# Kernel tuning notes

Hardware: AMD Instinct MI355X
Metric: run time of the kernel (lower is better)

## Reference

```python
import jax, jax.numpy as jnp
import numpy as np

N_NODES = 100000


def gcn_conv(x, W, b, src, dst, num_nodes):
    # PyG GCNConv: add self-loops, symmetric normalization, x @ W, scatter-add, + b
    xw = x @ W  # [N, out]
    loop = jnp.arange(num_nodes, dtype=src.dtype)
    s = jnp.concatenate([src, loop])  # message source j
    d = jnp.concatenate([dst, loop])  # aggregation target i
    deg = jax.ops.segment_sum(jnp.ones_like(d, dtype=xw.dtype), d, num_segments=num_nodes)
    dis = jnp.where(deg > 0, jax.lax.rsqrt(deg), 0.0)  # D^{-1/2}
    norm = dis[s] * dis[d]  # [E+N]
    msg = norm[:, None] * xw[s]  # gather + scale
    out = jax.ops.segment_sum(msg, d, num_segments=num_nodes)  # scatter-add
    return out + b


def setup_inputs() -> dict:
    key = jax.random.key(0)
    k1, k2, k3, k4 = jax.random.split(key, 4)
    F, H, E = 64, 64, 1250000
    x = jax.random.normal(k1, (N_NODES, F), dtype=jnp.float32)
    edge_index = jax.random.randint(k2, (2, E), 0, N_NODES, dtype=jnp.int64)
    W1 = jax.random.normal(k3, (F, H), dtype=jnp.float32) * (1.0 / np.sqrt(F))
    b1 = jnp.zeros((H,), dtype=jnp.float32)
    W2 = jax.random.normal(k4, (H, F), dtype=jnp.float32) * (1.0 / np.sqrt(H))
    b2 = jnp.zeros((F,), dtype=jnp.float32)
    return {"x": x, "edge_index": edge_index, "W1": W1, "b1": b1, "W2": W2, "b2": b2}


def reference(x, edge_index, W1, b1, W2, b2):
    src, dst = edge_index[0], edge_index[1]
    h = gcn_conv(x, W1, b1, src, dst, N_NODES)
    h = jax.nn.relu(h)
    out = gcn_conv(h, W2, b2, src, dst, N_NODES)
    return out
```

## Files before the change

### kernel.cpp

```cpp
#include <hip/hip_runtime.h>

#define NN    100000
#define F     64
#define NBUCK 391
#define CAPB  4096
#define TILE  4096
#define NBLKG 782
#define G1A   400

#define O_CURSOR 0
#define O_ROWPTR 512
#define O_DEG    100864
#define O_DIS    201216
#define O_PACKED 301568
#define O_SRT    1903104
#define O_AH     3504768
#define O_BH     6704768
#define O_W2F    9904768

typedef __attribute__((ext_vector_type(8))) short bf16x8;
typedef __attribute__((ext_vector_type(4))) float f32x4;

__device__ __forceinline__ unsigned bf_rne(float x) {
    unsigned u = __float_as_uint(x);
    return (u + 0x7FFFu + ((u >> 16) & 1u)) >> 16;
}
__device__ __forceinline__ unsigned pack2(float lo, float hi) {
    return bf_rne(lo) | (bf_rne(hi) << 16);
}
__device__ __forceinline__ float lo_f(unsigned u) { return __uint_as_float(u << 16); }
__device__ __forceinline__ float hi_f(unsigned u) { return __uint_as_float(u & 0xFFFF0000u); }

struct BpSmem {
    int hist[NBUCK], lofs[NBUCK], gbase[NBUCK], lcur[NBUCK];
    int wsum[8];
    unsigned stage[TILE];
    unsigned short sbuck[TILE];
};
union KSmem {
    BpSmem bp;
    unsigned w1f[16][64][4];
};
struct NsSmem {
    int h[256], lcur[256], wsum[4];
    int stage[CAPB];
};
union K2Smem {
    NsSmem ns;
    unsigned w1f[16][64][4];
};
struct K3Smem {
    unsigned w2f[16][64][4];
    unsigned hbuf[16 * 32];
    float dis_s[16];
};

__device__ __forceinline__ void binpack_body(const int* __restrict__ src,
                                             const int* __restrict__ dst, int E,
                                             int* __restrict__ cursor,
                                             unsigned* __restrict__ packed,
                                             int bid, BpSmem& sm) {
    int t  = threadIdx.x;
    int t0 = bid * TILE;
    int n  = min(TILE, E - t0);

    if (t < NBUCK) sm.hist[t] = 0;
    __syncthreads();
    int d_r[8], s_r[8];
#pragma unroll
    for (int it = 0; it < 8; ++it) {
        int i = t + it * 512;
        if (i < n) {
            d_r[it] = dst[t0 + i];
            s_r[it] = src[t0 + i];
            atomicAdd(&sm.hist[d_r[it] >> 8], 1);
        }
    }
    __syncthreads();
    int lane = t & 63, w = t >> 6;
    int v = (t < NBUCK) ? sm.hist[t] : 0;
    int s = v;
#pragma unroll
    for (int off = 1; off < 64; off <<= 1) {
        int u = __shfl_up(s, off, 64);
        if (lane >= off) s += u;
    }
    if (lane == 63) sm.wsum[w] = s;
    __syncthreads();
    if (t == 0) {
        int run = 0;
#pragma unroll
        for (int i = 0; i < 8; ++i) { int c = sm.wsum[i]; sm.wsum[i] = run; run += c; }
    }
    __syncthreads();
    if (t < NBUCK) {
        int ex = s - v + sm.wsum[w];
        sm.lofs[t] = ex;
        sm.lcur[t] = ex;
        sm.gbase[t] = t * CAPB + (v ? atomicAdd(&cursor[t], v) : 0);
    }
    __syncthreads();
#pragma unroll
    for (int it = 0; it < 8; ++it) {
        int i = t + it * 512;
        if (i < n) {
            int d = d_r[it];
            int b = d >> 8;
            int p = atomicAdd(&sm.lcur[b], 1);
            sm.stage[p] = ((unsigned)s_r[it] << 8) | (unsigned)(d & 255);
            sm.sbuck[p] = (unsigned short)b;
        }
    }
    __syncthreads();
    for (int i = t; i < n; i += 512) {
        int b = sm.sbuck[i];
        packed[sm.gbase[b] + (i - sm.lofs[b])] = sm.stage[i];
    }
}

__device__ __forceinline__ void gemm_mfma_body(const float* __restrict__ X,
                                               const float* __restrict__ W,
                                               unsigned* __restrict__ Ah, int bid,
                                               unsigned (*w1f)[64][4]) {
    int t = threadIdx.x;
    for (int idx = t; idx < 4096; idx += 512) {
        int slot = idx >> 8;
        int ks   = (slot >> 1) & 1;
        int p    = slot & 1;
        int ct   = slot >> 2;
        int l    = (idx >> 2) & 63;
        int j    = idx & 3;
        int k    = 32 * ks + 8 * (l >> 4) + 2 * j;
        int col  = 16 * ct + (l & 15);
        float v0 = W[k * 64 + col];
        float v1 = W[(k + 1) * 64 + col];
        if (p) {
            v0 -= __uint_as_float(bf_rne(v0) << 16);
            v1 -= __uint_as_float(bf_rne(v1) << 16);
        }
        ((unsigned*)w1f)[idx] = pack2(v0, v1);
    }

    int lane = t & 63, wid = t >> 6;
    int g = lane >> 4;
    int wrow0 = bid * 128 + wid * 16;
    int wrow  = wrow0 + (lane & 15);
    bool valid = wrow < NN;
    const float* xp = X + (size_t)wrow * F + 8 * g;
    float4 fz = {0.f, 0.f, 0.f, 0.f};
    float4 f0 = valid ? *(const float4*)(xp)      : fz;
    float4 f1 = valid ? *(const float4*)(xp + 4)  : fz;
    float4 f2 = valid ? *(const float4*)(xp + 32) : fz;
    float4 f3 = valid ? *(const float4*)(xp + 36) : fz;
    __syncthreads();

    f32x4 ac0 = {0.f,0.f,0.f,0.f}, ac1 = ac0, ac2 = ac0, ac3 = ac0;
#pragma unroll
    for (int ks = 0; ks < 2; ++ks) {
        float4 u0 = ks ? f2 : f0;
        float4 u1 = ks ? f3 : f1;
        uint4 hw;
        hw.x = pack2(u0.x, u0.y);
        hw.y = pack2(u0.z, u0.w);
        hw.z = pack2(u1.x, u1.y);
        hw.w = pack2(u1.z, u1.w);
        uint4 lw;
        lw.x = pack2(u0.x - lo_f(hw.x), u0.y - hi_f(hw.x));
        lw.y = pack2(u0.z - lo_f(hw.y), u0.w - hi_f(hw.y));
        lw.z = pack2(u1.x - lo_f(hw.z), u1.y - hi_f(hw.z));
        lw.w = pack2(u1.z - lo_f(hw.w), u1.w - hi_f(hw.w));
        bf16x8 Ahi = __builtin_bit_cast(bf16x8, hw);
        bf16x8 Alo = __builtin_bit_cast(bf16x8, lw);
#pragma unroll
        for (int ct = 0; ct < 4; ++ct) {
            uint4 bh = *(const uint4*)&w1f[ct * 4 + ks * 2 + 0][lane][0];
            uint4 bl = *(const uint4*)&w1f[ct * 4 + ks * 2 + 1][lane][0];
            bf16x8 Bh_ = __builtin_bit_cast(bf16x8, bh);
            bf16x8 Bl_ = __builtin_bit_cast(bf16x8, bl);
            f32x4& ac = (ct == 0) ? ac0 : (ct == 1) ? ac1 : (ct == 2) ? ac2 : ac3;
            ac = __builtin_amdgcn_mfma_f32_16x16x32_bf16(Ahi, Bh_, ac, 0, 0, 0);
            ac = __builtin_amdgcn_mfma_f32_16x16x32_bf16(Alo, Bh_, ac, 0, 0, 0);
            ac = __builtin_amdgcn_mfma_f32_16x16x32_bf16(Ahi, Bl_, ac, 0, 0, 0);
        }
    }
#pragma unroll
    for (int ct = 0; ct < 4; ++ct) {
        f32x4 ac = (ct == 0) ? ac0 : (ct == 1) ? ac1 : (ct == 2) ? ac2 : ac3;
#pragma unroll
        for (int r = 0; r < 4; ++r) {
            float val = ac[r];
            float q = __shfl_xor(val, 1, 64);
            int row = wrow0 + 4 * g + r;
            if (!(lane & 1) && row < NN) {
                int colp = 8 * ct + ((lane & 15) >> 1);
                Ah[(size_t)row * 32 + colp] = pack2(val, q);
            }
        }
    }
}

__device__ __forceinline__ void w2prep_body(const float* __restrict__ W2,
                                            unsigned* __restrict__ w2f) {
    int t = threadIdx.x;
    for (int idx = t; idx < 4096; idx += 512) {
        int slot = idx >> 8;
        int ks   = (slot >> 1) & 1;
        int p    = slot & 1;
        int ct   = slot >> 2;
        int l    = (idx >> 2) & 63;
        int j    = idx & 3;
        int k    = 32 * ks + 8 * (l >> 4) + 2 * j;
        int col  = 16 * ct + (l & 15);
        float v0 = W2[k * 64 + col];
        float v1 = W2[(k + 1) * 64 + col];
        if (p) {
            v0 -= __uint_as_float(bf_rne(v0) << 16);
            v1 -= __uint_as_float(bf_rne(v1) << 16);
        }
        w2f[idx] = pack2(v0, v1);
    }
}

__device__ __forceinline__ void node_sort_body(const unsigned* __restrict__ packed,
                                               const int* __restrict__ cursor,
                                               int* __restrict__ row_ptr,
                                               int* __restrict__ deg,
                                               float* __restrict__ dis,
                                               int* __restrict__ srt,
                                               int b, NsSmem& sm) {
    int t = threadIdx.x;
    int nbase = b << 8;
    int nloc = min(256, NN - nbase);
    int beg = b * CAPB;
    int n = cursor[b];

    if (t < 256) sm.h[t] = 0;
    __syncthreads();
    unsigned p_r[8];
#pragma unroll
    for (int it = 0; it < 8; ++it) {
        int i = t + it * 512;
        if (i < n) {
            p_r[it] = packed[beg + i];
            atomicAdd(&sm.h[p_r[it] & 255u], 1);
        }
    }
    __syncthreads();
    int lane = t & 63, w = t >> 6;
    int v = 0, s = 0;
    if (t < 256) { v = sm.h[t]; s = v; }
#pragma unroll
    for (int off = 1; off < 64; off <<= 1) {
        int u = __shfl_up(s, off, 64);
        if (lane >= off) s += u;
    }
    if (t < 256 && lane == 63) sm.wsum[w] = s;
    __syncthreads();
    if (t == 0) {
        int run = 0;
#pragma unroll
        for (int i = 0; i < 4; ++i) { int c = sm.wsum[i]; sm.wsum[i] = run; run += c; }
    }
    __syncthreads();
    if (t < 256) {
        int e0 = s - v + sm.wsum[w];
        sm.lcur[t] = e0;
        if (t < nloc) {
            row_ptr[nbase + t] = beg + e0;
            deg[nbase + t]     = v;
            dis[nbase + t]     = rsqrtf((float)v + 1.0f);
        }
    }
    __syncthreads();
#pragma unroll
    for (int it = 0; it < 8; ++it) {
        int i = t + it * 512;
        if (i < n) {
            unsigned p = p_r[it];
            int pos = atomicAdd(&sm.lcur[p & 255u], 1);
            sm.stage[pos] = (int)(p >> 8);
        }
    }
    __syncthreads();
    for (int i = t; i < n; i += 512) srt[beg + i] = sm.stage[i];
}

__global__ __launch_bounds__(512) void pre_gemm1(const int* __restrict__ src,
                                                 const int* __restrict__ dst, int E,
                                                 int nbp, int* __restrict__ cursor,
                                                 unsigned* __restrict__ packed,
                                                 const float* __restrict__ X,
                                                 const float* __restrict__ W1,
                                                 unsigned* __restrict__ Ah,
                                                 const float* __restrict__ W2,
                                                 unsigned* __restrict__ w2f) {
    __shared__ KSmem sm;
    if ((int)blockIdx.x < nbp)
        binpack_body(src, dst, E, cursor, packed, blockIdx.x, sm.bp);
    else if ((int)blockIdx.x < nbp + G1A)
        gemm_mfma_body(X, W1, Ah, (int)blockIdx.x - nbp, sm.w1f);
    else
        w2prep_body(W2, w2f);
}

__global__ __launch_bounds__(512) void sort_gemm1(const unsigned* __restrict__ packed,
                                                  const int* __restrict__ cursor,
                                                  int* __restrict__ row_ptr,
                                                  int* __restrict__ deg,
                                                  float* __restrict__ dis,
                                                  int* __restrict__ srt,
                                                  const float* __restrict__ X,
                                                  const float* __restrict__ W1,
                                                  unsigned* __restrict__ Ah) {
    __shared__ K2Smem sm;
    if ((int)blockIdx.x < NBUCK)
        node_sort_body(packed, cursor, row_ptr, deg, dis, srt, blockIdx.x, sm.ns);
    else
        gemm_mfma_body(X, W1, Ah, G1A + (int)blockIdx.x - NBUCK, sm.w1f);
}

__global__ __launch_bounds__(256) void agg1_gemm2(const uint4* __restrict__ Ah4,
                                                  const int* __restrict__ row_ptr,
                                                  const int* __restrict__ deg,
                                                  const int* __restrict__ srt,
                                                  const float* __restrict__ dis,
                                                  const float* __restrict__ b1,
                                                  const unsigned* __restrict__ w2fg,
                                                  unsigned* __restrict__ Bh) {
    __shared__ K3Smem sm;
    int t = threadIdx.x;
#pragma unroll
    for (int i = 0; i < 4; ++i)
        ((uint4*)sm.w2f)[t + 256 * i] = ((const uint4*)w2fg)[t + 256 * i];

    int sub  = t & 7;
    int grp  = (t >> 3) & 1;
    int node = blockIdx.x * 16 + (t >> 4);
    int beg = row_ptr[node];
    int end = beg + deg[node];
    float di = dis[node];

    float a0, a1, a2, a3, a4, a5, a6, a7;
    uint4 su = Ah4[(size_t)node * 8 + sub];
    if (grp == 0) {
        a0 = di * lo_f(su.x); a1 = di * hi_f(su.x);
        a2 = di * lo_f(su.y); a3 = di * hi_f(su.y);
        a4 = di * lo_f(su.z); a5 = di * hi_f(su.z);
        a6 = di * lo_f(su.w); a7 = di * hi_f(su.w);
    } else {
        a0 = a1 = a2 = a3 = a4 = a5 = a6 = a7 = 0.f;
    }

    int j = beg + grp;
    for (; j + 6 < end; j += 8) {
        int s0 = srt[j], s1 = srt[j + 2], s2 = srt[j + 4], s3 = srt[j + 6];
        float d0 = dis[s0], d1 = dis[s1], d2 = dis[s2], d3 = dis[s3];
        uint4 g0 = Ah4[(size_t)s0 * 8 + sub];
        uint4 g1 = Ah4[(size_t)s1 * 8 + sub];
        uint4 g2 = Ah4[(size_t)s2 * 8 + sub];
        uint4 g3 = Ah4[(size_t)s3 * 8 + sub];
        a0 = fmaf(d0, lo_f(g0.x), fmaf(d1, lo_f(g1.x), fmaf(d2, lo_f(g2.x), fmaf(d3, lo_f(g3.x), a0))));
        a1 = fmaf(d0, hi_f(g0.x), fmaf(d1, hi_f(g1.x), fmaf(d2, hi_f(g2.x), fmaf(d3, hi_f(g3.x), a1))));
        a2 = fmaf(d0, lo_f(g0.y), fmaf(d1, lo_f(g1.y), fmaf(d2, lo_f(g2.y), fmaf(d3, lo_f(g3.y), a2))));
        a3 = fmaf(d0, hi_f(g0.y), fmaf(d1, hi_f(g1.y), fmaf(d2, hi_f(g2.y), fmaf(d3, hi_f(g3.y), a3))));
        a4 = fmaf(d0, lo_f(g0.z), fmaf(d1, lo_f(g1.z), fmaf(d2, lo_f(g2.z), fmaf(d3, lo_f(g3.z), a4))));
        a5 = fmaf(d0, hi_f(g0.z), fmaf(d1, hi_f(g1.z), fmaf(d2, hi_f(g2.z), fmaf(d3, hi_f(g3.z), a5))));
        a6 = fmaf(d0, lo_f(g0.w), fmaf(d1, lo_f(g1.w), fmaf(d2, lo_f(g2.w), fmaf(d3, lo_f(g3.w), a6))));
        a7 = fmaf(d0, hi_f(g0.w), fmaf(d1, hi_f(g1.w), fmaf(d2, hi_f(g2.w), fmaf(d3, hi_f(g3.w), a7))));
    }
    for (; j + 2 < end; j += 4) {
        int s0 = srt[j], s1 = srt[j + 2];
        float d0 = dis[s0], d1 = dis[s1];
        uint4 g0 = Ah4[(size_t)s0 * 8 + sub];
        uint4 g1 = Ah4[(size_t)s1 * 8 + sub];
        a0 = fmaf(d0, lo_f(g0.x), fmaf(d1, lo_f(g1.x), a0));
        a1 = fmaf(d0, hi_f(g0.x), fmaf(d1, hi_f(g1.x), a1));
        a2 = fmaf(d0, lo_f(g0.y), fmaf(d1, lo_f(g1.y), a2));
        a3 = fmaf(d0, hi_f(g0.y), fmaf(d1, hi_f(g1.y), a3));
        a4 = fmaf(d0, lo_f(g0.z), fmaf(d1, lo_f(g1.z), a4));
        a5 = fmaf(d0, hi_f(g0.z), fmaf(d1, hi_f(g1.z), a5));
        a6 = fmaf(d0, lo_f(g0.w), fmaf(d1, lo_f(g1.w), a6));
        a7 = fmaf(d0, hi_f(g0.w), fmaf(d1, hi_f(g1.w), a7));
    }
    for (; j < end; j += 2) {
        int s0 = srt[j];
        float d0 = dis[s0];
        uint4 g0 = Ah4[(size_t)s0 * 8 + sub];
        a0 = fmaf(d0, lo_f(g0.x), a0);
        a1 = fmaf(d0, hi_f(g0.x), a1);
        a2 = fmaf(d0, lo_f(g0.y), a2);
        a3 = fmaf(d0, hi_f(g0.y), a3);
        a4 = fmaf(d0, lo_f(g0.z), a4);
        a5 = fmaf(d0, hi_f(g0.z), a5);
        a6 = fmaf(d0, lo_f(g0.w), a6);
        a7 = fmaf(d0, hi_f(g0.w), a7);
    }
    a0 += __shfl_xor(a0, 8, 64); a1 += __shfl_xor(a1, 8, 64);
    a2 += __shfl_xor(a2, 8, 64); a3 += __shfl_xor(a3, 8, 64);
    a4 += __shfl_xor(a4, 8, 64); a5 += __shfl_xor(a5, 8, 64);
    a6 += __shfl_xor(a6, 8, 64); a7 += __shfl_xor(a7, 8, 64);

    float4 bb0 = ((const float4*)b1)[2 * sub];
    float4 bb1 = ((const float4*)b1)[2 * sub + 1];
    float o0 = fmaxf(fmaf(di, a0, bb0.x), 0.f);
    float o1 = fmaxf(fmaf(di, a1, bb0.y), 0.f);
    float o2 = fmaxf(fmaf(di, a2, bb0.z), 0.f);
    float o3 = fmaxf(fmaf(di, a3, bb0.w), 0.f);
    float o4 = fmaxf(fmaf(di, a4, bb1.x), 0.f);
    float o5 = fmaxf(fmaf(di, a5, bb1.y), 0.f);
    float o6 = fmaxf(fmaf(di, a6, bb1.z), 0.f);
    float o7 = fmaxf(fmaf(di, a7, bb1.w), 0.f);

    int node15 = t >> 4;
    if (!(t & 8)) {
        int unit = sub ^ (node15 & 7);
        uint4 hv;
        hv.x = pack2(o0, o1);
        hv.y = pack2(o2, o3);
        hv.z = pack2(o4, o5);
        hv.w = pack2(o6, o7);
        *(uint4*)&sm.hbuf[node15 * 32 + unit * 4] = hv;
        if (sub == 0) sm.dis_s[node15] = di;
    }
    __syncthreads();

    int lane = t & 63, ct = t >> 6;
    int row = lane & 15, g = lane >> 4;
    f32x4 acc = {0.f, 0.f, 0.f, 0.f};
#pragma unroll
    for (int ks = 0; ks < 2; ++ks) {
        int unit = (4 * ks + g) ^ (row & 7);
        uint4 araw = *(const uint4*)&sm.hbuf[row * 32 + unit * 4];
        uint4 bhr  = *(const uint4*)&sm.w2f[ct * 4 + ks * 2 + 0][lane][0];
        uint4 blr  = *(const uint4*)&sm.w2f[ct * 4 + ks * 2 + 1][lane][0];
        bf16x8 A  = __builtin_bit_cast(bf16x8, araw);
        bf16x8 Bh_ = __builtin_bit_cast(bf16x8, bhr);
        bf16x8 Bl_ = __builtin_bit_cast(bf16x8, blr);
        acc = __builtin_amdgcn_mfma_f32_16x16x32_bf16(A, Bh_, acc, 0, 0, 0);
        acc = __builtin_amdgcn_mfma_f32_16x16x32_bf16(A, Bl_, acc, 0, 0, 0);
    }
    int nbase16 = blockIdx.x * 16;
#pragma unroll
    for (int r = 0; r < 4; ++r) {
        int nd = 4 * g + r;
        float val = acc[r] * sm.dis_s[nd];
        float q = __shfl_xor(val, 1, 64);
        if (!(lane & 1)) {
            int colp = 8 * ct + ((lane & 15) >> 1);
            Bh[(size_t)(nbase16 + nd) * 32 + colp] = pack2(val, q);
        }
    }
}

__global__ __launch_bounds__(256) void agg_out(const uint4* __restrict__ Bs4,
                                               const int* __restrict__ row_ptr,
                                               const int* __restrict__ deg,
                                               const int* __restrict__ srt,
                                               const float* __restrict__ dis,
                                               const float* __restrict__ bias,
                                               float* __restrict__ outp) {
    int t = threadIdx.x;
    int sub  = t & 7;
    int grp  = (t >> 3) & 1;
    int node = blockIdx.x * 16 + (t >> 4);
    int beg = row_ptr[node];
    int end = beg + deg[node];
    float di = dis[node];

    float a0, a1, a2, a3, a4, a5, a6, a7;
    uint4 su = Bs4[(size_t)node * 8 + sub];
    if (grp == 0) {
        a0 = lo_f(su.x); a1 = hi_f(su.x);
        a2 = lo_f(su.y); a3 = hi_f(su.y);
        a4 = lo_f(su.z); a5 = hi_f(su.z);
        a6 = lo_f(su.w); a7 = hi_f(su.w);
    } else {
        a0 = a1 = a2 = a3 = a4 = a5 = a6 = a7 = 0.f;
    }

    int j = beg + grp;
    for (; j + 6 < end; j += 8) {
        int s0 = srt[j], s1 = srt[j + 2], s2 = srt[j + 4], s3 = srt[j + 6];
        uint4 g0 = Bs4[(size_t)s0 * 8 + sub];
        uint4 g1 = Bs4[(size_t)s1 * 8 + sub];
        uint4 g2 = Bs4[(size_t)s2 * 8 + sub];
        uint4 g3 = Bs4[(size_t)s3 * 8 + sub];
        a0 += (lo_f(g0.x) + lo_f(g1.x)) + (lo_f(g2.x) + lo_f(g3.x));
        a1 += (hi_f(g0.x) + hi_f(g1.x)) + (hi_f(g2.x) + hi_f(g3.x));
        a2 += (lo_f(g0.y) + lo_f(g1.y)) + (lo_f(g2.y) + lo_f(g3.y));
        a3 += (hi_f(g0.y) + hi_f(g1.y)) + (hi_f(g2.y) + hi_f(g3.y));
        a4 += (lo_f(g0.z) + lo_f(g1.z)) + (lo_f(g2.z) + lo_f(g3.z));
        a5 += (hi_f(g0.z) + hi_f(g1.z)) + (hi_f(g2.z) + hi_f(g3.z));
        a6 += (lo_f(g0.w) + lo_f(g1.w)) + (lo_f(g2.w) + lo_f(g3.w));
        a7 += (hi_f(g0.w) + hi_f(g1.w)) + (hi_f(g2.w) + hi_f(g3.w));
    }
    for (; j + 2 < end; j += 4) {
        int s0 = srt[j], s1 = srt[j + 2];
        uint4 g0 = Bs4[(size_t)s0 * 8 + sub];
        uint4 g1 = Bs4[(size_t)s1 * 8 + sub];
        a0 += lo_f(g0.x) + lo_f(g1.x);
        a1 += hi_f(g0.x) + hi_f(g1.x);
        a2 += lo_f(g0.y) + lo_f(g1.y);
        a3 += hi_f(g0.y) + hi_f(g1.y);
        a4 += lo_f(g0.z) + lo_f(g1.z);
        a5 += hi_f(g0.z) + hi_f(g1.z);
        a6 += lo_f(g0.w) + lo_f(g1.w);
        a7 += hi_f(g0.w) + hi_f(g1.w);
    }
    for (; j < end; j += 2) {
        int s0 = srt[j];
        uint4 g0 = Bs4[(size_t)s0 * 8 + sub];
        a0 += lo_f(g0.x); a1 += hi_f(g0.x);
        a2 += lo_f(g0.y); a3 += hi_f(g0.y);
        a4 += lo_f(g0.z); a5 += hi_f(g0.z);
        a6 += lo_f(g0.w); a7 += hi_f(g0.w);
    }
    a0 += __shfl_xor(a0, 8, 64); a1 += __shfl_xor(a1, 8, 64);
    a2 += __shfl_xor(a2, 8, 64); a3 += __shfl_xor(a3, 8, 64);
    a4 += __shfl_xor(a4, 8, 64); a5 += __shfl_xor(a5, 8, 64);
    a6 += __shfl_xor(a6, 8, 64); a7 += __shfl_xor(a7, 8, 64);

    float4 bb0 = ((const float4*)bias)[2 * sub];
    float4 bb1 = ((const float4*)bias)[2 * sub + 1];
    float4 o;
    if (grp == 0) {
        o.x = fmaf(di, a0, bb0.x);
        o.y = fmaf(di, a1, bb0.y);
        o.z = fmaf(di, a2, bb0.z);
        o.w = fmaf(di, a3, bb0.w);
        ((float4*)outp)[(size_t)node * 16 + 2 * sub] = o;
    } else {
        o.x = fmaf(di, a4, bb1.x);
        o.y = fmaf(di, a5, bb1.y);
        o.z = fmaf(di, a6, bb1.z);
        o.w = fmaf(di, a7, bb1.w);
        ((float4*)outp)[(size_t)node * 16 + 2 * sub + 1] = o;
    }
}

extern "C" void kernel_launch(void* const* d_in, const int* in_sizes, int n_in,
                              void* d_out, int out_size, void* d_ws, size_t ws_size,
                              hipStream_t stream) {
    const float* x  = (const float*)d_in[0];
    const int*   ei = (const int*)d_in[1];
    const float* W1 = (const float*)d_in[2];
    const float* b1 = (const float*)d_in[3];
    const float* W2 = (const float*)d_in[4];
    const float* b2 = (const float*)d_in[5];
    float* out = (float*)d_out;
    int E = in_sizes[1] / 2;
    const int* src = ei;
    const int* dst = ei + E;

    int*      ws_i    = (int*)d_ws;
    int*      cursor  = ws_i + O_CURSOR;
    int*      row_ptr = ws_i + O_ROWPTR;
    int*      deg     = ws_i + O_DEG;
    float*    dis     = (float*)(ws_i + O_DIS);
    unsigned* packed  = (unsigned*)(ws_i + O_PACKED);
    int*      srt     = ws_i + O_SRT;
    unsigned* Ah      = (unsigned*)(ws_i + O_AH);
    unsigned* Bh      = (unsigned*)(ws_i + O_BH);
    unsigned* w2f     = (unsigned*)(ws_i + O_W2F);

    int nbp = (E + TILE - 1) / TILE;

    (void)hipMemsetAsync(cursor, 0, NBUCK * sizeof(int), stream);
    pre_gemm1<<<nbp + G1A + 1, 512, 0, stream>>>(src, dst, E, nbp, cursor, packed,
                                                 x, W1, Ah, W2, w2f);
    sort_gemm1<<<NBUCK + (NBLKG - G1A), 512, 0, stream>>>(packed, cursor, row_ptr,
                                                          deg, dis, srt, x, W1, Ah);
    agg1_gemm2<<<NN / 16, 256, 0, stream>>>((const uint4*)Ah, row_ptr, deg, srt,
                                            dis, b1, w2f, Bh);
    agg_out<<<NN / 16, 256, 0, stream>>>((const uint4*)Bh, row_ptr, deg, srt,
                                         dis, b2, out);
}
```

Baseline: 182.7 us.

## Store pre-scaled byte offsets in CSR, pad rows, split neighbor halves, packed FMA

The node sort now stores each neighbor as a byte offset (source index shifted left by 7) and pads each node's segment to an even length. This allows 8-byte aligned int2 index loads and removes the address multiply in the gather loops. The aggregation kernels split each node's neighbor list into contiguous halves per lane group instead of interleaving them, and accumulate with two-wide float vectors so the compiler can emit packed FMA and add instructions. The price is slightly more sort storage and a one-bit precondition: the shifted offsets must fit in an int and are shifted back to look up dis.

```diff
diff --git a/kernel.cpp b/kernel.cpp
--- a/kernel.cpp
+++ b/kernel.cpp
@@ -20,6 +20,7 @@
 
 typedef __attribute__((ext_vector_type(8))) short bf16x8;
 typedef __attribute__((ext_vector_type(4))) float f32x4;
+typedef __attribute__((ext_vector_type(2))) float f32x2;
 
 __device__ __forceinline__ unsigned bf_rne(float x) {
     unsigned u = __float_as_uint(x);
@@ -30,6 +31,10 @@
 }
 __device__ __forceinline__ float lo_f(unsigned u) { return __uint_as_float(u << 16); }
 __device__ __forceinline__ float hi_f(unsigned u) { return __uint_as_float(u & 0xFFFF0000u); }
+__device__ __forceinline__ f32x2 up2(unsigned u) {
+    f32x2 r = {__uint_as_float(u << 16), __uint_as_float(u & 0xFFFF0000u)};
+    return r;
+}
 
 struct BpSmem {
     int hist[NBUCK], lofs[NBUCK], gbase[NBUCK], lcur[NBUCK];
@@ -42,7 +47,7 @@
     unsigned w1f[16][64][4];
 };
 struct NsSmem {
-    int h[256], lcur[256], wsum[4];
+    int h[256], lcur[256], wsum[4], ptot;
     int stage[CAPB];
 };
 union K2Smem {
@@ -247,8 +252,8 @@
     }
     __syncthreads();
     int lane = t & 63, w = t >> 6;
-    int v = 0, s = 0;
-    if (t < 256) { v = sm.h[t]; s = v; }
+    int v = 0, pd = 0, s = 0;
+    if (t < 256) { v = sm.h[t]; pd = (v + 1) & ~1; s = pd; }
 #pragma unroll
     for (int off = 1; off < 64; off <<= 1) {
         int u = __shfl_up(s, off, 64);
@@ -263,13 +268,14 @@
     }
     __syncthreads();
     if (t < 256) {
-        int e0 = s - v + sm.wsum[w];
+        int e0 = s - pd + sm.wsum[w];
         sm.lcur[t] = e0;
         if (t < nloc) {
             row_ptr[nbase + t] = beg + e0;
             deg[nbase + t]     = v;
             dis[nbase + t]     = rsqrtf((float)v + 1.0f);
         }
+        if (t == nloc - 1) sm.ptot = e0 + pd;
     }
     __syncthreads();
 #pragma unroll
@@ -278,11 +284,12 @@
         if (i < n) {
             unsigned p = p_r[it];
             int pos = atomicAdd(&sm.lcur[p & 255u], 1);
-            sm.stage[pos] = (int)(p >> 8);
-        }
-    }
-    __syncthreads();
-    for (int i = t; i < n; i += 512) srt[beg + i] = sm.stage[i];
+            sm.stage[pos] = (int)((p >> 8) << 7);
+        }
+    }
+    __syncthreads();
+    int ptot = sm.ptot;
+    for (int i = t; i < ptot; i += 512) srt[beg + i] = sm.stage[i];
 }
 
 __global__ __launch_bounds__(512) void pre_gemm1(const int* __restrict__ src,
@@ -319,7 +326,7 @@
         gemm_mfma_body(X, W1, Ah, G1A + (int)blockIdx.x - NBUCK, sm.w1f);
 }
 
-__global__ __launch_bounds__(256) void agg1_gemm2(const uint4* __restrict__ Ah4,
+__global__ __launch_bounds__(256) void agg1_gemm2(const unsigned* __restrict__ AhW,
                                                   const int* __restrict__ row_ptr,
                                                   const int* __restrict__ deg,
                                                   const int* __restrict__ srt,
@@ -333,68 +340,86 @@
     for (int i = 0; i < 4; ++i)
         ((uint4*)sm.w2f)[t + 256 * i] = ((const uint4*)w2fg)[t + 256 * i];
 
+    const char* baseA = (const char*)AhW;
     int sub  = t & 7;
     int grp  = (t >> 3) & 1;
+    int soff = sub * 16;
     int node = blockIdx.x * 16 + (t >> 4);
+    int cnt = deg[node];
     int beg = row_ptr[node];
-    int end = beg + deg[node];
     float di = dis[node];
 
-    float a0, a1, a2, a3, a4, a5, a6, a7;
-    uint4 su = Ah4[(size_t)node * 8 + sub];
+    f32x2 A0, A1, A2, A3;
     if (grp == 0) {
-        a0 = di * lo_f(su.x); a1 = di * hi_f(su.x);
-        a2 = di * lo_f(su.y); a3 = di * hi_f(su.y);
-        a4 = di * lo_f(su.z); a5 = di * hi_f(su.z);
-        a6 = di * lo_f(su.w); a7 = di * hi_f(su.w);
+        uint4 su = *(const uint4*)(baseA + ((size_t)node * 128 + soff));
+        A0 = f32x2{di * lo_f(su.x), di * hi_f(su.x)};
+        A1 = f32x2{di * lo_f(su.y), di * hi_f(su.y)};
+        A2 = f32x2{di * lo_f(su.z), di * hi_f(su.z)};
+        A3 = f32x2{di * lo_f(su.w), di * hi_f(su.w)};
     } else {
-        a0 = a1 = a2 = a3 = a4 = a5 = a6 = a7 = 0.f;
-    }
-
-    int j = beg + grp;
-    for (; j + 6 < end; j += 8) {
-        int s0 = srt[j], s1 = srt[j + 2], s2 = srt[j + 4], s3 = srt[j + 6];
-        float d0 = dis[s0], d1 = dis[s1], d2 = dis[s2], d3 = dis[s3];
-        uint4 g0 = Ah4[(size_t)s0 * 8 + sub];
-        uint4 g1 = Ah4[(size_t)s1 * 8 + sub];
-        uint4 g2 = Ah4[(size_t)s2 * 8 + sub];
-        uint4 g3 = Ah4[(size_t)s3 * 8 + sub];
-        a0 = fmaf(d0, lo_f(g0.x), fmaf(d1, lo_f(g1.x), fmaf(d2, lo_f(g2.x), fmaf(d3, lo_f(g3.x), a0))));
-        a1 = fmaf(d0, hi_f(g0.x), fmaf(d1, hi_f(g1.x), fmaf(d2, hi_f(g2.x), fmaf(d3, hi_f(g3.x), a1))));
-        a2 = fmaf(d0, lo_f(g0.y), fmaf(d1, lo_f(g1.y), fmaf(d2, lo_f(g2.y), fmaf(d3, lo_f(g3.y), a2))));
-        a3 = fmaf(d0, hi_f(g0.y), fmaf(d1, hi_f(g1.y), fmaf(d2, hi_f(g2.y), fmaf(d3, hi_f(g3.y), a3))));
-        a4 = fmaf(d0, lo_f(g0.z), fmaf(d1, lo_f(g1.z), fmaf(d2, lo_f(g2.z), fmaf(d3, lo_f(g3.z), a4))));
-        a5 = fmaf(d0, hi_f(g0.z), fmaf(d1, hi_f(g1.z), fmaf(d2, hi_f(g2.z), fmaf(d3, hi_f(g3.z), a5))));
-        a6 = fmaf(d0, lo_f(g0.w), fmaf(d1, lo_f(g1.w), fmaf(d2, lo_f(g2.w), fmaf(d3, lo_f(g3.w), a6))));
-        a7 = fmaf(d0, hi_f(g0.w), fmaf(d1, hi_f(g1.w), fmaf(d2, hi_f(g2.w), fmaf(d3, hi_f(g3.w), a7))));
-    }
-    for (; j + 2 < end; j += 4) {
-        int s0 = srt[j], s1 = srt[j + 2];
-        float d0 = dis[s0], d1 = dis[s1];
-        uint4 g0 = Ah4[(size_t)s0 * 8 + sub];
-        uint4 g1 = Ah4[(size_t)s1 * 8 + sub];
-        a0 = fmaf(d0, lo_f(g0.x), fmaf(d1, lo_f(g1.x), a0));
-        a1 = fmaf(d0, hi_f(g0.x), fmaf(d1, hi_f(g1.x), a1));
-        a2 = fmaf(d0, lo_f(g0.y), fmaf(d1, lo_f(g1.y), a2));
-        a3 = fmaf(d0, hi_f(g0.y), fmaf(d1, hi_f(g1.y), a3));
-        a4 = fmaf(d0, lo_f(g0.z), fmaf(d1, lo_f(g1.z), a4));
-        a5 = fmaf(d0, hi_f(g0.z), fmaf(d1, hi_f(g1.z), a5));
-        a6 = fmaf(d0, lo_f(g0.w), fmaf(d1, lo_f(g1.w), a6));
-        a7 = fmaf(d0, hi_f(g0.w), fmaf(d1, hi_f(g1.w), a7));
-    }
-    for (; j < end; j += 2) {
-        int s0 = srt[j];
-        float d0 = dis[s0];
-        uint4 g0 = Ah4[(size_t)s0 * 8 + sub];
-        a0 = fmaf(d0, lo_f(g0.x), a0);
-        a1 = fmaf(d0, hi_f(g0.x), a1);
-        a2 = fmaf(d0, lo_f(g0.y), a2);
-        a3 = fmaf(d0, hi_f(g0.y), a3);
-        a4 = fmaf(d0, lo_f(g0.z), a4);
-        a5 = fmaf(d0, hi_f(g0.z), a5);
-        a6 = fmaf(d0, lo_f(g0.w), a6);
-        a7 = fmaf(d0, hi_f(g0.w), a7);
-    }
+        A0 = A1 = A2 = A3 = f32x2{0.f, 0.f};
+    }
+
+    int h  = min(cnt, ((cnt >> 1) + 1) & ~1);
+    int jb = beg + (grp ? h : 0);
+    int je = jb + (grp ? (cnt - h) : h);
+    for (; jb + 4 <= je; jb += 4) {
+        int2 sa = *(const int2*)&srt[jb];
+        int2 sb = *(const int2*)&srt[jb + 2];
+        float d0 = dis[(unsigned)sa.x >> 7];
+        float d1 = dis[(unsigned)sa.y >> 7];
+        float d2 = dis[(unsigned)sb.x >> 7];
+        float d3 = dis[(unsigned)sb.y >> 7];
+        uint4 g0 = *(const uint4*)(baseA + (sa.x + soff));
+        uint4 g1 = *(const uint4*)(baseA + (sa.y + soff));
+        uint4 g2 = *(const uint4*)(baseA + (sb.x + soff));
+        uint4 g3 = *(const uint4*)(baseA + (sb.y + soff));
+        f32x2 dd0 = {d0, d0}, dd1 = {d1, d1}, dd2 = {d2, d2}, dd3 = {d3, d3};
+        A0 = __builtin_elementwise_fma(dd0, up2(g0.x), A0);
+        A1 = __builtin_elementwise_fma(dd0, up2(g0.y), A1);
+        A2 = __builtin_elementwise_fma(dd0, up2(g0.z), A2);
+        A3 = __builtin_elementwise_fma(dd0, up2(g0.w), A3);
+        A0 = __builtin_elementwise_fma(dd1, up2(g1.x), A0);
+        A1 = __builtin_elementwise_fma(dd1, up2(g1.y), A1);
+        A2 = __builtin_elementwise_fma(dd1, up2(g1.z), A2);
+        A3 = __builtin_elementwise_fma(dd1, up2(g1.w), A3);
+        A0 = __builtin_elementwise_fma(dd2, up2(g2.x), A0);
+        A1 = __builtin_elementwise_fma(dd2, up2(g2.y), A1);
+        A2 = __builtin_elementwise_fma(dd2, up2(g2.z), A2);
+        A3 = __builtin_elementwise_fma(dd2, up2(g2.w), A3);
+        A0 = __builtin_elementwise_fma(dd3, up2(g3.x), A0);
+        A1 = __builtin_elementwise_fma(dd3, up2(g3.y), A1);
+        A2 = __builtin_elementwise_fma(dd3, up2(g3.z), A2);
+        A3 = __builtin_elementwise_fma(dd3, up2(g3.w), A3);
+    }
+    for (; jb + 2 <= je; jb += 2) {
+        int2 sa = *(const int2*)&srt[jb];
+        float d0 = dis[(unsigned)sa.x >> 7];
+        float d1 = dis[(unsigned)sa.y >> 7];
+        uint4 g0 = *(const uint4*)(baseA + (sa.x + soff));
+        uint4 g1 = *(const uint4*)(baseA + (sa.y + soff));
+        f32x2 dd0 = {d0, d0}, dd1 = {d1, d1};
+        A0 = __builtin_elementwise_fma(dd0, up2(g0.x), A0);
+        A1 = __builtin_elementwise_fma(dd0, up2(g0.y), A1);
+        A2 = __builtin_elementwise_fma(dd0, up2(g0.z), A2);
+        A3 = __builtin_elementwise_fma(dd0, up2(g0.w), A3);
+        A0 = __builtin_elementwise_fma(dd1, up2(g1.x), A0);
+        A1 = __builtin_elementwise_fma(dd1, up2(g1.y), A1);
+        A2 = __builtin_elementwise_fma(dd1, up2(g1.z), A2);
+        A3 = __builtin_elementwise_fma(dd1, up2(g1.w), A3);
+    }
+    if (jb < je) {
+        int sa = srt[jb];
+        float d0 = dis[(unsigned)sa >> 7];
+        uint4 g0 = *(const uint4*)(baseA + (sa + soff));
+        f32x2 dd0 = {d0, d0};
+        A0 = __builtin_elementwise_fma(dd0, up2(g0.x), A0);
+        A1 = __builtin_elementwise_fma(dd0, up2(g0.y), A1);
+        A2 = __builtin_elementwise_fma(dd0, up2(g0.z), A2);
+        A3 = __builtin_elementwise_fma(dd0, up2(g0.w), A3);
+    }
+    float a0 = A0.x, a1 = A0.y, a2 = A1.x, a3 = A1.y;
+    float a4 = A2.x, a5 = A2.y, a6 = A3.x, a7 = A3.y;
     a0 += __shfl_xor(a0, 8, 64); a1 += __shfl_xor(a1, 8, 64);
     a2 += __shfl_xor(a2, 8, 64); a3 += __shfl_xor(a3, 8, 64);
     a4 += __shfl_xor(a4, 8, 64); a5 += __shfl_xor(a5, 8, 64);
@@ -452,7 +477,7 @@
     }
 }
 
-__global__ __launch_bounds__(256) void agg_out(const uint4* __restrict__ Bs4,
+__global__ __launch_bounds__(256) void agg_out(const unsigned* __restrict__ BsW,
                                                const int* __restrict__ row_ptr,
                                                const int* __restrict__ deg,
                                                const int* __restrict__ srt,
@@ -460,61 +485,57 @@
                                                const float* __restrict__ bias,
                                                float* __restrict__ outp) {
     int t = threadIdx.x;
+    const char* baseB = (const char*)BsW;
     int sub  = t & 7;
     int grp  = (t >> 3) & 1;
+    int soff = sub * 16;
     int node = blockIdx.x * 16 + (t >> 4);
+    int cnt = deg[node];
     int beg = row_ptr[node];
-    int end = beg + deg[node];
     float di = dis[node];
 
-    float a0, a1, a2, a3, a4, a5, a6, a7;
-    uint4 su = Bs4[(size_t)node * 8 + sub];
+    f32x2 A0, A1, A2, A3;
     if (grp == 0) {
-        a0 = lo_f(su.x); a1 = hi_f(su.x);
-        a2 = lo_f(su.y); a3 = hi_f(su.y);
-        a4 = lo_f(su.z); a5 = hi_f(su.z);
-        a6 = lo_f(su.w); a7 = hi_f(su.w);
+        uint4 su = *(const uint4*)(baseB + ((size_t)node * 128 + soff));
+        A0 = up2(su.x); A1 = up2(su.y); A2 = up2(su.z); A3 = up2(su.w);
     } else {
-        a0 = a1 = a2 = a3 = a4 = a5 = a6 = a7 = 0.f;
-    }
-
-    int j = beg + grp;
-    for (; j + 6 < end; j += 8) {
-        int s0 = srt[j], s1 = srt[j + 2], s2 = srt[j + 4], s3 = srt[j + 6];
-        uint4 g0 = Bs4[(size_t)s0 * 8 + sub];
-        uint4 g1 = Bs4[(size_t)s1 * 8 + sub];
-        uint4 g2 = Bs4[(size_t)s2 * 8 + sub];
-        uint4 g3 = Bs4[(size_t)s3 * 8 + sub];
-        a0 += (lo_f(g0.x) + lo_f(g1.x)) + (lo_f(g2.x) + lo_f(g3.x));
-        a1 += (hi_f(g0.x) + hi_f(g1.x)) + (hi_f(g2.x) + hi_f(g3.x));
-        a2 += (lo_f(g0.y) + lo_f(g1.y)) + (lo_f(g2.y) + lo_f(g3.y));
-        a3 += (hi_f(g0.y) + hi_f(g1.y)) + (hi_f(g2.y) + hi_f(g3.y));
-        a4 += (lo_f(g0.z) + lo_f(g1.z)) + (lo_f(g2.z) + lo_f(g3.z));
-        a5 += (hi_f(g0.z) + hi_f(g1.z)) + (hi_f(g2.z) + hi_f(g3.z));
-        a6 += (lo_f(g0.w) + lo_f(g1.w)) + (lo_f(g2.w) + lo_f(g3.w));
-        a7 += (hi_f(g0.w) + hi_f(g1.w)) + (hi_f(g2.w) + hi_f(g3.w));
-    }
-    for (; j + 2 < end; j += 4) {
-        int s0 = srt[j], s1 = srt[j + 2];
-        uint4 g0 = Bs4[(size_t)s0 * 8 + sub];
-        uint4 g1 = Bs4[(size_t)s1 * 8 + sub];
-        a0 += lo_f(g0.x) + lo_f(g1.x);
-        a1 += hi_f(g0.x) + hi_f(g1.x);
-        a2 += lo_f(g0.y) + lo_f(g1.y);
-        a3 += hi_f(g0.y) + hi_f(g1.y);
-        a4 += lo_f(g0.z) + lo_f(g1.z);
-        a5 += hi_f(g0.z) + hi_f(g1.z);
-        a6 += lo_f(g0.w) + lo_f(g1.w);
-        a7 += hi_f(g0.w) + hi_f(g1.w);
-    }
-    for (; j < end; j += 2) {
-        int s0 = srt[j];
-        uint4 g0 = Bs4[(size_t)s0 * 8 + sub];
-        a0 += lo_f(g0.x); a1 += hi_f(g0.x);
-        a2 += lo_f(g0.y); a3 += hi_f(g0.y);
-        a4 += lo_f(g0.z); a5 += hi_f(g0.z);
-        a6 += lo_f(g0.w); a7 += hi_f(g0.w);
-    }
+        A0 = A1 = A2 = A3 = f32x2{0.f, 0.f};
+    }
+
+    int h  = min(cnt, ((cnt >> 1) + 1) & ~1);
+    int jb = beg + (grp ? h : 0);
+    int je = jb + (grp ? (cnt - h) : h);
+    for (; jb + 4 <= je; jb += 4) {
+        int2 sa = *(const int2*)&srt[jb];
+        int2 sb = *(const int2*)&srt[jb + 2];
+        uint4 g0 = *(const uint4*)(baseB + (sa.x + soff));
+        uint4 g1 = *(const uint4*)(baseB + (sa.y + soff));
+        uint4 g2 = *(const uint4*)(baseB + (sb.x + soff));
+        uint4 g3 = *(const uint4*)(baseB + (sb.y + soff));
+        A0 = A0 + (up2(g0.x) + up2(g1.x)) + (up2(g2.x) + up2(g3.x));
+        A1 = A1 + (up2(g0.y) + up2(g1.y)) + (up2(g2.y) + up2(g3.y));
+        A2 = A2 + (up2(g0.z) + up2(g1.z)) + (up2(g2.z) + up2(g3.z));
+        A3 = A3 + (up2(g0.w) + up2(g1.w)) + (up2(g2.w) + up2(g3.w));
+    }
+    for (; jb + 2 <= je; jb += 2) {
+        int2 sa = *(const int2*)&srt[jb];
+        uint4 g0 = *(const uint4*)(baseB + (sa.x + soff));
+        uint4 g1 = *(const uint4*)(baseB + (sa.y + soff));
+        A0 = A0 + up2(g0.x) + up2(g1.x);
+        A1 = A1 + up2(g0.y) + up2(g1.y);
+        A2 = A2 + up2(g0.z) + up2(g1.z);
+        A3 = A3 + up2(g0.w) + up2(g1.w);
+    }
+    if (jb < je) {
+        int sa = srt[jb];
+        uint4 g0 = *(const uint4*)(baseB + (sa + soff));
+        A0 = A0 + up2(g0.x);
+        A1 = A1 + up2(g0.y);
+        A2 = A2 + up2(g0.z);
+        A3 = A3 + up2(g0.w);
+    }
+    float a0 = A0.x, a1 = A0.y, a2 = A1.x, a3 = A1.y;
+    float a4 = A2.x, a5 = A2.y, a6 = A3.x, a7 = A3.y;
     a0 += __shfl_xor(a0, 8, 64); a1 += __shfl_xor(a1, 8, 64);
     a2 += __shfl_xor(a2, 8, 64); a3 += __shfl_xor(a3, 8, 64);
     a4 += __shfl_xor(a4, 8, 64); a5 += __shfl_xor(a5, 8, 64);
@@ -570,8 +591,8 @@
                                                  x, W1, Ah, W2, w2f);
     sort_gemm1<<<NBUCK + (NBLKG - G1A), 512, 0, stream>>>(packed, cursor, row_ptr,
                                                           deg, dis, srt, x, W1, Ah);
-    agg1_gemm2<<<NN / 16, 256, 0, stream>>>((const uint4*)Ah, row_ptr, deg, srt,
+    agg1_gemm2<<<NN / 16, 256, 0, stream>>>(Ah, row_ptr, deg, srt,
                                             dis, b1, w2f, Bh);
-    agg_out<<<NN / 16, 256, 0, stream>>>((const uint4*)Bh, row_ptr, deg, srt,
+    agg_out<<<NN / 16, 256, 0, stream>>>(Bh, row_ptr, deg, srt,
                                          dis, b2, out);
 }
```

Result: no change. 181.2 us (median of 2 runs) (-0.9%).
